# Performance work log

Hardware: AMD Instinct MI355X
Metric: run time of the kernel (lower is better)

The kernel has to match this reference:

```python
import jax, jax.numpy as jnp
import numpy as np
from jax import lax

START = 0  # label_dict['<START>']
END = 8    # label_dict['<END>']
NEG = -10000.0


def setup_inputs() -> dict:
    key = jax.random.key(0)
    k1, k2, k3 = jax.random.split(key, 3)
    B, S, C = 8192, 512, 9
    emission = jax.random.normal(k1, (B, S, C), dtype=jnp.float32)
    # transition_matrix ~ normal, then START row / END column masked to -10000
    T = jax.random.normal(k2, (C, C), dtype=jnp.float32)
    T = T.at[START, :].set(NEG).at[:, END].set(NEG)
    labels = jax.random.randint(k3, (B, S), 0, 8, dtype=jnp.int32)
    mask = jnp.ones((B, S), dtype=jnp.int32)
    return {"emission": emission, "transition": T, "labels": labels, "mask": mask}


def _log_partition(emission, T, mask_f):
    # emission: [B,S,C], T: [C,C], mask_f: [B,S] float
    B, S, C = emission.shape
    init = jnp.full((B, C), NEG, dtype=emission.dtype).at[:, 0].set(0.0)

    def step(log_alpha, inp):
        em_t, m_t = inp  # [B,C], [B,1]
        # add[b,i,j] = log_alpha[b,i] + em_t[b,j] + T[i,j]
        add = log_alpha[:, :, None] + em_t[:, None, :] + T[None, :, :]
        new = jax.nn.logsumexp(add, axis=1)  # [B,C]
        log_alpha = new * m_t + log_alpha * (1.0 - m_t)
        return log_alpha, None

    em_sw = jnp.swapaxes(emission, 0, 1)          # [S,B,C]
    m_sw = jnp.swapaxes(mask_f, 0, 1)[:, :, None]  # [S,B,1]
    final, _ = lax.scan(step, init, (em_sw, m_sw))
    final = final + T[:, END][None, :]
    return jax.nn.logsumexp(final, axis=1)  # [B]


def _sentence_score(emission, T, labels, mask_f):
    B, S, C = emission.shape
    # prepend <START>=0 label
    labels_ext = jnp.concatenate(
        [jnp.full((B, 1), START, dtype=labels.dtype), labels], axis=1)  # [B,S+1]
    # emission score at the gold label of each position
    emit = jnp.take_along_axis(emission, labels[:, :, None].astype(jnp.int32), axis=2)[..., 0]  # [B,S]
    trans = T[labels_ext[:, :-1], labels_ext[:, 1:]]  # [B,S]
    scores = jnp.sum((emit + trans) * mask_f, axis=1)  # [B]
    lengths = jnp.sum(mask_f, axis=1).astype(jnp.int32)  # [B]
    last_label = labels_ext[jnp.arange(B), lengths]       # label at position len in ext seq
    scores = scores + T[last_label, END]
    return scores


def reference(emission, transition, labels, mask):
    mask_f = mask.astype(emission.dtype)
    log_Z = _log_partition(emission, transition, mask_f)
    gold = _sentence_score(emission, transition, labels, mask_f)
    loss = jnp.mean(log_Z - gold)
    return loss
```

## Files before the change

### kernel.cpp

```cpp
#include <hip/hip_runtime.h>


#define CC 9
#define SS 512
#define NEGV (-10000.0f)
#define BLOCKT 256
#define BPW 8
#define BPB 32

template <int M>
__device__ __forceinline__ float rotf(float v) {
    return __int_as_float(__builtin_amdgcn_update_dpp(
        0, __float_as_int(v), 0x120 + 2 * M, 0xF, 0xF, false));
}
template <int M>
__device__ __forceinline__ int roti(int v) {
    return __builtin_amdgcn_update_dpp(0, v, 0x120 + 2 * M, 0xF, 0xF, false);
}

struct Chunk {
    float em[8];
    int lab[8];
    int msk[8];
};

struct St {
    float q, offset, goldtr, goldem;
    int len, prev;
};

__device__ __forceinline__ void load_chunk(Chunk& c, const float* emp,
                                           const int* labp, const int* mskp, int t0) {
#pragma unroll
    for (int k = 0; k < 8; ++k) c.em[k] = emp[(t0 + k) * CC];
    int4 l0 = *(const int4*)(labp + t0);
    int4 l1 = *(const int4*)(labp + t0 + 4);
    int4 m0 = *(const int4*)(mskp + t0);
    int4 m1 = *(const int4*)(mskp + t0 + 4);
    c.lab[0] = l0.x; c.lab[1] = l0.y; c.lab[2] = l0.z; c.lab[3] = l0.w;
    c.lab[4] = l1.x; c.lab[5] = l1.y; c.lab[6] = l1.z; c.lab[7] = l1.w;
    c.msk[0] = m0.x; c.msk[1] = m0.y; c.msk[2] = m0.z; c.msk[3] = m0.w;
    c.msk[4] = m1.x; c.msk[5] = m1.y; c.msk[6] = m1.z; c.msk[7] = m1.w;
}

template <bool RENORM>
__device__ __forceinline__ void crf_step(St& st, float e, float em, int lab, int msk,
                                         float tv, const float* w, int o) {
    float q = st.q;
    float g1 = rotf<1>(q), g2 = rotf<2>(q), g3 = rotf<3>(q);
    float g4 = rotf<4>(q), g5 = rotf<5>(q), g6 = rotf<6>(q), g7 = rotf<7>(q);
    float s0 = q * w[0];
    float s1 = g1 * w[1];
    float s2 = g2 * w[2];
    s0 = fmaf(g3, w[3], s0);
    s1 = fmaf(g4, w[4], s1);
    s2 = fmaf(g5, w[5], s2);
    s0 = fmaf(g6, w[6], s0);
    s1 = fmaf(g7, w[7], s1);
    float ssum = s0 + (s1 + s2);
    bool m = (msk != 0);
    st.goldtr += m ? tv : 0.0f;
    st.goldem += (m && lab == o) ? em : 0.0f;
    st.len += m ? 1 : 0;
    float nq = m ? ssum * e : q;
    if (RENORM) {
        float mx = fmaxf(nq, rotf<1>(nq));
        mx = fmaxf(mx, rotf<2>(mx));
        mx = fmaxf(mx, rotf<4>(mx));
        nq *= __builtin_amdgcn_rcpf(mx);
        st.offset += __logf(mx);
    }
    st.q = nq;
}

__device__ __forceinline__ void consume8(St& st, const Chunk& c, const float* Tl,
                                         const float* w, int o) {
    float tv[8];
    tv[0] = Tl[st.prev * CC + c.lab[0]];
#pragma unroll
    for (int k = 1; k < 8; ++k) tv[k] = Tl[c.lab[k - 1] * CC + c.lab[k]];
    st.prev = c.lab[7];
    float e[8];
#pragma unroll
    for (int k = 0; k < 8; ++k) e[k] = __expf(c.em[k]);
    crf_step<true >(st, e[0], c.em[0], c.lab[0], c.msk[0], tv[0], w, o);
    crf_step<false>(st, e[1], c.em[1], c.lab[1], c.msk[1], tv[1], w, o);
    crf_step<false>(st, e[2], c.em[2], c.lab[2], c.msk[2], tv[2], w, o);
    crf_step<false>(st, e[3], c.em[3], c.lab[3], c.msk[3], tv[3], w, o);
    crf_step<true >(st, e[4], c.em[4], c.lab[4], c.msk[4], tv[4], w, o);
    crf_step<false>(st, e[5], c.em[5], c.lab[5], c.msk[5], tv[5], w, o);
    crf_step<false>(st, e[6], c.em[6], c.lab[6], c.msk[6], tv[6], w, o);
    crf_step<false>(st, e[7], c.em[7], c.lab[7], c.msk[7], tv[7], w, o);
}

__global__ __launch_bounds__(BLOCKT, 1) void crf_main(
    const float* __restrict__ emission, const float* __restrict__ transition,
    const int* __restrict__ labels, const int* __restrict__ mask,
    float* __restrict__ out, int B, float invB) {
    __shared__ float Tl[CC * CC];
    __shared__ float blocksum;
    int tid = threadIdx.x;
    if (tid == 0) blocksum = 0.0f;
    for (int i = tid; i < CC * CC; i += BLOCKT) Tl[i] = transition[i];
    __syncthreads();

    int lane = tid & 63, wv = tid >> 6;
    int pos = lane & 15, row = lane >> 4;
    int par = pos & 1, s = pos >> 1;
    int o = s;
    long batch = (long)blockIdx.x * BPB + wv * BPW + row * 2 + par;
    bool valid = batch < (long)B;
    size_t bidx = valid ? (size_t)batch : 0;

    int ssrc[8];
    ssrc[0] = s;
    ssrc[1] = roti<1>(s); ssrc[2] = roti<2>(s); ssrc[3] = roti<3>(s);
    ssrc[4] = roti<4>(s); ssrc[5] = roti<5>(s); ssrc[6] = roti<6>(s);
    ssrc[7] = roti<7>(s);
    float wmain[8], wf[8];
#pragma unroll
    for (int m = 0; m < 8; ++m) {
        int is_ = ssrc[m];
        wmain[m] = __expf(Tl[is_ * CC + o]);
        wf[m] = __expf(Tl[(is_ == 0 ? 8 : is_) * CC + o]);
    }

    float mT8 = Tl[8];
#pragma unroll
    for (int i = 1; i < CC; ++i) mT8 = fmaxf(mT8, Tl[i * CC + 8]);
    float wend = __expf(Tl[o * CC + 8] - mT8);

    int colq = (s == 0) ? 8 : s;
    float v, vref;
    {
        float mx1 = Tl[colq], mx2 = Tl[1];
#pragma unroll
        for (int i = 1; i < CC; ++i) {
            mx1 = fmaxf(mx1, NEGV + Tl[i * CC + colq]);
            mx2 = fmaxf(mx2, NEGV + Tl[i * CC + 1]);
        }
        float a1 = __expf(Tl[colq] - mx1), a2 = __expf(Tl[1] - mx2);
#pragma unroll
        for (int i = 1; i < CC; ++i) {
            a1 += __expf(NEGV + Tl[i * CC + colq] - mx1);
            a2 += __expf(NEGV + Tl[i * CC + 1] - mx2);
        }
        v = mx1 + __logf(a1);
        vref = mx2 + __logf(a2);
    }

    const float* emp = emission + bidx * (SS * CC) + o;
    const int* labp = labels + bidx * SS;
    const int* mskp = mask + bidx * SS;
    float em8 = emission[bidx * (SS * CC) + 8];

    Chunk A, Bc;
    load_chunk(A, emp, labp, mskp, 0);
    load_chunk(Bc, emp, labp, mskp, 8);

    St st;
    st.q = 0.f; st.offset = 0.f; st.goldtr = 0.f; st.goldem = 0.f;
    st.len = 0; st.prev = 0;

    {
        bool m0 = (A.msk[0] != 0);
        float em0q = (s == 0) ? em8 : A.em[0];
        st.q = m0 ? __expf(v + em0q - vref) : 0.0f;
        st.offset = m0 ? vref : 0.0f;
        st.goldtr = m0 ? Tl[A.lab[0]] : 0.0f;
        st.goldem = (m0 && A.lab[0] == o) ? A.em[0] : 0.0f;
        st.len = m0 ? 1 : 0;
    }
    {
        float tv[8];
#pragma unroll
        for (int k = 1; k < 8; ++k) tv[k] = Tl[A.lab[k - 1] * CC + A.lab[k]];
        st.prev = A.lab[7];
        float e[8];
#pragma unroll
        for (int k = 1; k < 8; ++k) e[k] = __expf(A.em[k]);
        crf_step<false>(st, e[1], A.em[1], A.lab[1], A.msk[1], tv[1], wf, o);
        crf_step<false>(st, e[2], A.em[2], A.lab[2], A.msk[2], tv[2], wmain, o);
        crf_step<false>(st, e[3], A.em[3], A.lab[3], A.msk[3], tv[3], wmain, o);
        crf_step<true >(st, e[4], A.em[4], A.lab[4], A.msk[4], tv[4], wmain, o);
        crf_step<false>(st, e[5], A.em[5], A.lab[5], A.msk[5], tv[5], wmain, o);
        crf_step<false>(st, e[6], A.em[6], A.lab[6], A.msk[6], tv[6], wmain, o);
        crf_step<false>(st, e[7], A.em[7], A.lab[7], A.msk[7], tv[7], wmain, o);
    }
    load_chunk(A, emp, labp, mskp, 16);

    for (int c = 1; c <= 61; c += 2) {
        consume8(st, Bc, Tl, wmain, o);
        load_chunk(Bc, emp, labp, mskp, (c + 2) * 8);
        consume8(st, A, Tl, wmain, o);
        if (c + 3 <= 63) load_chunk(A, emp, labp, mskp, (c + 3) * 8);
    }
    consume8(st, Bc, Tl, wmain, o);

    int lastlab = (st.len > 0) ? labp[st.len - 1] : 0;
    float gend = Tl[lastlab * CC + 8];
    float fin = st.q * wend;
    float sw = fin + rotf<1>(fin);
    sw = sw + rotf<2>(sw);
    sw = sw + rotf<4>(sw);
    float gpart = st.goldem + ((s == 0) ? (st.goldtr + gend) : 0.0f);
    float sg = gpart + rotf<1>(gpart);
    sg = sg + rotf<2>(sg);
    sg = sg + rotf<4>(sg);
    if (valid && s == 0) {
        float logZ = st.offset + mT8 + __logf(sw);
        atomicAdd(&blocksum, (logZ - sg) * invB);
    }
    __syncthreads();
    if (tid == 0) atomicAdd(out, blocksum);
}

extern "C" void kernel_launch(void* const* d_in, const int* in_sizes, int n_in,
                              void* d_out, int out_size, void* d_ws, size_t ws_size,
                              hipStream_t stream) {
    const float* emission = (const float*)d_in[0];
    const float* transition = (const float*)d_in[1];
    const int* labels = (const int*)d_in[2];
    const int* mask = (const int*)d_in[3];
    float* out = (float*)d_out;

    int B = in_sizes[2] / SS;
    float invB = 1.0f / (float)B;

    hipMemsetAsync(out, 0, sizeof(float) * out_size, stream);
    int nblocks = (B + BPB - 1) / BPB;
    crf_main<<<nblocks, BLOCKT, 0, stream>>>(emission, transition, labels, mask,
                                             out, B, invB);
}
```

Baseline: 246.6 us.

## Split CRF recursion into forward and backward halves run by paired waves

Each sequence's partition-function recursion is split at the midpoint. One wave runs the forward alpha recursion over the first 256 steps. A second wave runs a backward beta recursion over the last 256 steps. The two are combined through shared memory with a dot product of alpha and beta. This halves the serial dependency chain per sequence and raises occupancy by halving batches per block and allowing two blocks per CU. It adds shared-memory exchange and a block barrier, and the backward path's handling of partial masks is less obviously correct than the forward-only version.

```diff
diff --git a/kernel.cpp b/kernel.cpp
--- a/kernel.cpp
+++ b/kernel.cpp
@@ -5,8 +5,10 @@
 #define SS 512
 #define NEGV (-10000.0f)
 #define BLOCKT 256
+#define HALF 256
+#define NCH 32
 #define BPW 8
-#define BPB 32
+#define BPB 16
 
 template <int M>
 __device__ __forceinline__ float rotf(float v) {
@@ -22,6 +24,7 @@
     float em[8];
     int lab[8];
     int msk[8];
+    int labm1;
 };
 
 struct St {
@@ -41,6 +44,20 @@
     c.lab[4] = l1.x; c.lab[5] = l1.y; c.lab[6] = l1.z; c.lab[7] = l1.w;
     c.msk[0] = m0.x; c.msk[1] = m0.y; c.msk[2] = m0.z; c.msk[3] = m0.w;
     c.msk[4] = m1.x; c.msk[5] = m1.y; c.msk[6] = m1.z; c.msk[7] = m1.w;
+}
+
+__device__ __forceinline__ void load_chunk_b(Chunk& c, const float* emp,
+                                             const int* labp, const int* mskp, int t0) {
+    load_chunk(c, emp, labp, mskp, t0);
+    c.labm1 = labp[t0 - 1];
+}
+
+__device__ __forceinline__ void renorm8(St& st, float& nq) {
+    float mx = fmaxf(nq, rotf<1>(nq));
+    mx = fmaxf(mx, rotf<2>(mx));
+    mx = fmaxf(mx, rotf<4>(mx));
+    nq *= __builtin_amdgcn_rcpf(mx);
+    st.offset += __logf(mx);
 }
 
 template <bool RENORM>
@@ -63,13 +80,32 @@
     st.goldem += (m && lab == o) ? em : 0.0f;
     st.len += m ? 1 : 0;
     float nq = m ? ssum * e : q;
-    if (RENORM) {
-        float mx = fmaxf(nq, rotf<1>(nq));
-        mx = fmaxf(mx, rotf<2>(mx));
-        mx = fmaxf(mx, rotf<4>(mx));
-        nq *= __builtin_amdgcn_rcpf(mx);
-        st.offset += __logf(mx);
-    }
+    if (RENORM) renorm8(st, nq);
+    st.q = nq;
+}
+
+template <bool RENORM>
+__device__ __forceinline__ void crf_step_b(St& st, float e, float em, int lab, int msk,
+                                           float tv, const float* w, int o) {
+    float q = st.q;
+    float p = q * e;
+    float g1 = rotf<1>(p), g2 = rotf<2>(p), g3 = rotf<3>(p);
+    float g4 = rotf<4>(p), g5 = rotf<5>(p), g6 = rotf<6>(p), g7 = rotf<7>(p);
+    float s0 = p * w[0];
+    float s1 = g1 * w[1];
+    float s2 = g2 * w[2];
+    s0 = fmaf(g3, w[3], s0);
+    s1 = fmaf(g4, w[4], s1);
+    s2 = fmaf(g5, w[5], s2);
+    s0 = fmaf(g6, w[6], s0);
+    s1 = fmaf(g7, w[7], s1);
+    float ssum = s0 + (s1 + s2);
+    bool m = (msk != 0);
+    st.goldtr += m ? tv : 0.0f;
+    st.goldem += (m && lab == o) ? em : 0.0f;
+    st.len += m ? 1 : 0;
+    float nq = m ? ssum : q;
+    if (RENORM) renorm8(st, nq);
     st.q = nq;
 }
 
@@ -93,11 +129,34 @@
     crf_step<false>(st, e[7], c.em[7], c.lab[7], c.msk[7], tv[7], w, o);
 }
 
-__global__ __launch_bounds__(BLOCKT, 1) void crf_main(
+__device__ __forceinline__ void consume8_b(St& st, const Chunk& c, const float* Tl,
+                                           const float* w, int o) {
+    float tv[8];
+    tv[0] = Tl[c.labm1 * CC + c.lab[0]];
+#pragma unroll
+    for (int k = 1; k < 8; ++k) tv[k] = Tl[c.lab[k - 1] * CC + c.lab[k]];
+    float e[8];
+#pragma unroll
+    for (int k = 0; k < 8; ++k) e[k] = __expf(c.em[k]);
+    crf_step_b<true >(st, e[7], c.em[7], c.lab[7], c.msk[7], tv[7], w, o);
+    crf_step_b<false>(st, e[6], c.em[6], c.lab[6], c.msk[6], tv[6], w, o);
+    crf_step_b<false>(st, e[5], c.em[5], c.lab[5], c.msk[5], tv[5], w, o);
+    crf_step_b<false>(st, e[4], c.em[4], c.lab[4], c.msk[4], tv[4], w, o);
+    crf_step_b<true >(st, e[3], c.em[3], c.lab[3], c.msk[3], tv[3], w, o);
+    crf_step_b<false>(st, e[2], c.em[2], c.lab[2], c.msk[2], tv[2], w, o);
+    crf_step_b<false>(st, e[1], c.em[1], c.lab[1], c.msk[1], tv[1], w, o);
+    crf_step_b<false>(st, e[0], c.em[0], c.lab[0], c.msk[0], tv[0], w, o);
+}
+
+__global__ __launch_bounds__(BLOCKT, 2) void crf_main(
     const float* __restrict__ emission, const float* __restrict__ transition,
     const int* __restrict__ labels, const int* __restrict__ mask,
     float* __restrict__ out, int B, float invB) {
     __shared__ float Tl[CC * CC];
+    __shared__ float su[BPB][8];
+    __shared__ float soff[BPB];
+    __shared__ float sgold[BPB];
+    __shared__ int slen[BPB];
     __shared__ float blocksum;
     int tid = threadIdx.x;
     if (tid == 0) blocksum = 0.0f;
@@ -108,7 +167,9 @@
     int pos = lane & 15, row = lane >> 4;
     int par = pos & 1, s = pos >> 1;
     int o = s;
-    long batch = (long)blockIdx.x * BPB + wv * BPW + row * 2 + par;
+    int isB = wv & 1;
+    int lb = (wv >> 1) * BPW + row * 2 + par;
+    long batch = (long)blockIdx.x * BPB + lb;
     bool valid = batch < (long)B;
     size_t bidx = valid ? (size_t)batch : 0;
 
@@ -117,100 +178,143 @@
     ssrc[1] = roti<1>(s); ssrc[2] = roti<2>(s); ssrc[3] = roti<3>(s);
     ssrc[4] = roti<4>(s); ssrc[5] = roti<5>(s); ssrc[6] = roti<6>(s);
     ssrc[7] = roti<7>(s);
-    float wmain[8], wf[8];
-#pragma unroll
-    for (int m = 0; m < 8; ++m) {
-        int is_ = ssrc[m];
-        wmain[m] = __expf(Tl[is_ * CC + o]);
-        wf[m] = __expf(Tl[(is_ == 0 ? 8 : is_) * CC + o]);
-    }
-
-    float mT8 = Tl[8];
-#pragma unroll
-    for (int i = 1; i < CC; ++i) mT8 = fmaxf(mT8, Tl[i * CC + 8]);
-    float wend = __expf(Tl[o * CC + 8] - mT8);
-
-    int colq = (s == 0) ? 8 : s;
-    float v, vref;
-    {
-        float mx1 = Tl[colq], mx2 = Tl[1];
-#pragma unroll
-        for (int i = 1; i < CC; ++i) {
-            mx1 = fmaxf(mx1, NEGV + Tl[i * CC + colq]);
-            mx2 = fmaxf(mx2, NEGV + Tl[i * CC + 1]);
-        }
-        float a1 = __expf(Tl[colq] - mx1), a2 = __expf(Tl[1] - mx2);
-#pragma unroll
-        for (int i = 1; i < CC; ++i) {
-            a1 += __expf(NEGV + Tl[i * CC + colq] - mx1);
-            a2 += __expf(NEGV + Tl[i * CC + 1] - mx2);
-        }
-        v = mx1 + __logf(a1);
-        vref = mx2 + __logf(a2);
-    }
 
     const float* emp = emission + bidx * (SS * CC) + o;
     const int* labp = labels + bidx * SS;
     const int* mskp = mask + bidx * SS;
-    float em8 = emission[bidx * (SS * CC) + 8];
-
-    Chunk A, Bc;
-    load_chunk(A, emp, labp, mskp, 0);
-    load_chunk(Bc, emp, labp, mskp, 8);
-
-    St st;
-    st.q = 0.f; st.offset = 0.f; st.goldtr = 0.f; st.goldem = 0.f;
-    st.len = 0; st.prev = 0;
-
-    {
-        bool m0 = (A.msk[0] != 0);
-        float em0q = (s == 0) ? em8 : A.em[0];
-        st.q = m0 ? __expf(v + em0q - vref) : 0.0f;
-        st.offset = m0 ? vref : 0.0f;
-        st.goldtr = m0 ? Tl[A.lab[0]] : 0.0f;
-        st.goldem = (m0 && A.lab[0] == o) ? A.em[0] : 0.0f;
-        st.len = m0 ? 1 : 0;
+
+    if (!isB) {
+        float wmain[8], wf[8];
+#pragma unroll
+        for (int m = 0; m < 8; ++m) {
+            int is_ = ssrc[m];
+            wmain[m] = __expf(Tl[is_ * CC + o]);
+            wf[m] = __expf(Tl[(is_ == 0 ? 8 : is_) * CC + o]);
+        }
+
+        int colq = (s == 0) ? 8 : s;
+        float v, vref;
+        {
+            float mx1 = Tl[colq], mx2 = Tl[1];
+#pragma unroll
+            for (int i = 1; i < CC; ++i) {
+                mx1 = fmaxf(mx1, NEGV + Tl[i * CC + colq]);
+                mx2 = fmaxf(mx2, NEGV + Tl[i * CC + 1]);
+            }
+            float a1 = __expf(Tl[colq] - mx1), a2 = __expf(Tl[1] - mx2);
+#pragma unroll
+            for (int i = 1; i < CC; ++i) {
+                a1 += __expf(NEGV + Tl[i * CC + colq] - mx1);
+                a2 += __expf(NEGV + Tl[i * CC + 1] - mx2);
+            }
+            v = mx1 + __logf(a1);
+            vref = mx2 + __logf(a2);
+        }
+        float em8 = emission[bidx * (SS * CC) + 8];
+
+        Chunk A, Bc;
+        load_chunk(A, emp, labp, mskp, 0);
+        load_chunk(Bc, emp, labp, mskp, 8);
+
+        St st;
+        st.q = 0.f; st.offset = 0.f; st.goldtr = 0.f; st.goldem = 0.f;
+        st.len = 0; st.prev = 0;
+
+        {
+            bool m0 = (A.msk[0] != 0);
+            float em0q = (s == 0) ? em8 : A.em[0];
+            st.q = m0 ? __expf(v + em0q - vref) : 0.0f;
+            st.offset = m0 ? vref : 0.0f;
+            st.goldtr = m0 ? Tl[A.lab[0]] : 0.0f;
+            st.goldem = (m0 && A.lab[0] == o) ? A.em[0] : 0.0f;
+            st.len = m0 ? 1 : 0;
+        }
+        {
+            float tv[8];
+#pragma unroll
+            for (int k = 1; k < 8; ++k) tv[k] = Tl[A.lab[k - 1] * CC + A.lab[k]];
+            st.prev = A.lab[7];
+            float e[8];
+#pragma unroll
+            for (int k = 1; k < 8; ++k) e[k] = __expf(A.em[k]);
+            crf_step<false>(st, e[1], A.em[1], A.lab[1], A.msk[1], tv[1], wf, o);
+            crf_step<false>(st, e[2], A.em[2], A.lab[2], A.msk[2], tv[2], wmain, o);
+            crf_step<false>(st, e[3], A.em[3], A.lab[3], A.msk[3], tv[3], wmain, o);
+            crf_step<true >(st, e[4], A.em[4], A.lab[4], A.msk[4], tv[4], wmain, o);
+            crf_step<false>(st, e[5], A.em[5], A.lab[5], A.msk[5], tv[5], wmain, o);
+            crf_step<false>(st, e[6], A.em[6], A.lab[6], A.msk[6], tv[6], wmain, o);
+            crf_step<false>(st, e[7], A.em[7], A.lab[7], A.msk[7], tv[7], wmain, o);
+        }
+        load_chunk(A, emp, labp, mskp, 16);
+
+        for (int c = 1; c <= NCH - 3; c += 2) {
+            consume8(st, Bc, Tl, wmain, o);
+            load_chunk(Bc, emp, labp, mskp, (c + 2) * 8);
+            consume8(st, A, Tl, wmain, o);
+            if (c + 3 <= NCH - 1) load_chunk(A, emp, labp, mskp, (c + 3) * 8);
+        }
+        consume8(st, Bc, Tl, wmain, o);
+
+        su[lb][s] = st.q;
+        float gpart = st.goldem + ((s == 0) ? st.goldtr : 0.0f);
+        float sg = gpart + rotf<1>(gpart);
+        sg = sg + rotf<2>(sg);
+        sg = sg + rotf<4>(sg);
+        if (s == 0) {
+            soff[lb] = st.offset;
+            sgold[lb] = sg;
+            slen[lb] = st.len;
+        }
+    } else {
+        float wb[8];
+#pragma unroll
+        for (int m = 0; m < 8; ++m) wb[m] = __expf(Tl[o * CC + ssrc[m]]);
+
+        float mT8 = Tl[8];
+#pragma unroll
+        for (int i = 1; i < CC; ++i) mT8 = fmaxf(mT8, Tl[i * CC + 8]);
+
+        St st;
+        st.q = __expf(Tl[o * CC + 8] - mT8);
+        st.offset = mT8;
+        st.goldtr = 0.f; st.goldem = 0.f; st.len = 0; st.prev = 0;
+
+        Chunk A, Bc;
+        load_chunk_b(A, emp, labp, mskp, HALF + 8 * (NCH - 1));
+        load_chunk_b(Bc, emp, labp, mskp, HALF + 8 * (NCH - 2));
+        consume8_b(st, A, Tl, wb, o);
+        load_chunk_b(A, emp, labp, mskp, HALF + 8 * (NCH - 3));
+
+        for (int cc = NCH - 2; cc >= 2; cc -= 2) {
+            consume8_b(st, Bc, Tl, wb, o);
+            load_chunk_b(Bc, emp, labp, mskp, HALF + 8 * (cc - 2));
+            consume8_b(st, A, Tl, wb, o);
+            if (cc - 3 >= 0) load_chunk_b(A, emp, labp, mskp, HALF + 8 * (cc - 3));
+        }
+        consume8_b(st, Bc, Tl, wb, o);
+
+        __syncthreads();
+        float u = su[lb][s];
+        float prodv = u * st.q;
+        float sw = prodv + rotf<1>(prodv);
+        sw = sw + rotf<2>(sw);
+        sw = sw + rotf<4>(sw);
+        int lenT = slen[lb] + st.len;
+        float gpart = st.goldem;
+        if (s == 0) {
+            int lastlab = (lenT > 0) ? labp[lenT - 1] : 0;
+            gpart += st.goldtr + Tl[lastlab * CC + 8];
+        }
+        float sg = gpart + rotf<1>(gpart);
+        sg = sg + rotf<2>(sg);
+        sg = sg + rotf<4>(sg);
+        if (valid && s == 0) {
+            float logZ = soff[lb] + st.offset + __logf(sw);
+            float gold = sgold[lb] + sg;
+            atomicAdd(&blocksum, (logZ - gold) * invB);
+        }
     }
-    {
-        float tv[8];
-#pragma unroll
-        for (int k = 1; k < 8; ++k) tv[k] = Tl[A.lab[k - 1] * CC + A.lab[k]];
-        st.prev = A.lab[7];
-        float e[8];
-#pragma unroll
-        for (int k = 1; k < 8; ++k) e[k] = __expf(A.em[k]);
-        crf_step<false>(st, e[1], A.em[1], A.lab[1], A.msk[1], tv[1], wf, o);
-        crf_step<false>(st, e[2], A.em[2], A.lab[2], A.msk[2], tv[2], wmain, o);
-        crf_step<false>(st, e[3], A.em[3], A.lab[3], A.msk[3], tv[3], wmain, o);
-        crf_step<true >(st, e[4], A.em[4], A.lab[4], A.msk[4], tv[4], wmain, o);
-        crf_step<false>(st, e[5], A.em[5], A.lab[5], A.msk[5], tv[5], wmain, o);
-        crf_step<false>(st, e[6], A.em[6], A.lab[6], A.msk[6], tv[6], wmain, o);
-        crf_step<false>(st, e[7], A.em[7], A.lab[7], A.msk[7], tv[7], wmain, o);
-    }
-    load_chunk(A, emp, labp, mskp, 16);
-
-    for (int c = 1; c <= 61; c += 2) {
-        consume8(st, Bc, Tl, wmain, o);
-        load_chunk(Bc, emp, labp, mskp, (c + 2) * 8);
-        consume8(st, A, Tl, wmain, o);
-        if (c + 3 <= 63) load_chunk(A, emp, labp, mskp, (c + 3) * 8);
-    }
-    consume8(st, Bc, Tl, wmain, o);
-
-    int lastlab = (st.len > 0) ? labp[st.len - 1] : 0;
-    float gend = Tl[lastlab * CC + 8];
-    float fin = st.q * wend;
-    float sw = fin + rotf<1>(fin);
-    sw = sw + rotf<2>(sw);
-    sw = sw + rotf<4>(sw);
-    float gpart = st.goldem + ((s == 0) ? (st.goldtr + gend) : 0.0f);
-    float sg = gpart + rotf<1>(gpart);
-    sg = sg + rotf<2>(sg);
-    sg = sg + rotf<4>(sg);
-    if (valid && s == 0) {
-        float logZ = st.offset + mT8 + __logf(sw);
-        atomicAdd(&blocksum, (logZ - sg) * invB);
-    }
+    if (!isB) __syncthreads();
     __syncthreads();
     if (tid == 0) atomicAdd(out, blocksum);
 }
```

After: 248.4 us. Within noise of the previous version (+0.7%).
